# Kernel optimization log

Measured on AMD Instinct MI355X. Metric: run time of the kernel, lower is better.

The kernel has to match this reference:

```python
import jax, jax.numpy as jnp
import numpy as np

N_NODES = 50000
N_EDGES = 1600000
N_FEAT = 512
N_HID = 256
N_CLS = 64
K_HOPS = 10
ALPHA = 0.1


def setup_inputs() -> dict:
    key = jax.random.key(0)
    k1, k2, k3, k4 = jax.random.split(key, 4)
    x = jax.random.normal(k1, (N_NODES, N_FEAT), dtype=jnp.float32)
    edge_index = jax.random.randint(k2, (2, N_EDGES), 0, N_NODES, dtype=jnp.int64)
    W1 = jax.random.normal(k3, (N_HID, N_FEAT), dtype=jnp.float32) * (1.0 / np.sqrt(N_FEAT))
    W2 = jax.random.normal(k4, (N_CLS, N_HID), dtype=jnp.float32) * (1.0 / np.sqrt(N_HID))
    return {"x": x, "edge_index": edge_index, "W1": W1, "W2": W2}


def reference(x, edge_index, W1, W2):
    n = x.shape[0]
    # --- MLP encoder (eval mode: dropout is identity) ---
    hidden = jax.nn.relu(x @ W1.T)            # [N, n_hidden]
    out = hidden @ W2.T                        # [N, n_classes]

    # --- GCN normalization with self-loops (PyG gcn_norm defaults) ---
    loops = jnp.arange(n, dtype=edge_index.dtype)
    src = jnp.concatenate([edge_index[0], loops])  # [E+N]
    dst = jnp.concatenate([edge_index[1], loops])  # [E+N]
    deg = jax.ops.segment_sum(jnp.ones_like(src, dtype=out.dtype), dst, num_segments=n)
    dinv = jnp.where(deg > 0, jax.lax.rsqrt(deg), 0.0)
    norm = dinv[src] * dinv[dst]                   # [E+N]

    # --- APPNP: K hops of propagate + teleport blend ---
    h0 = out
    for _ in range(K_HOPS):
        msg = norm[:, None] * out[src]                         # gather [E+N, C]
        agg = jax.ops.segment_sum(msg, dst, num_segments=n)    # scatter-add [N, C]
        out = (1.0 - ALPHA) * agg + ALPHA * h0

    return jax.nn.log_softmax(out, axis=1)
```

## Files before the change

kernel.cpp:

```cpp
#include <hip/hip_runtime.h>
#include <hip/hip_bf16.h>
#include <cstdint>
#include <cstddef>

#define N_NODES 50000
#define N_EDGES 1600000
#define N_FEAT  512
#define N_HID   256
#define N_CLS   64
#define K_HOPS  10
#define NPAD    50016
#define DUMMY   N_NODES
#define P16(d) (((d) + 15) & ~15)
#define STAGE_CAP 256
#define HOP_GRID 3125
#define NPS 6250

typedef __attribute__((ext_vector_type(4))) float f32x4;
typedef __attribute__((ext_vector_type(4))) int   i32x4;
typedef __attribute__((ext_vector_type(2))) unsigned int u32x2;
typedef __attribute__((ext_vector_type(4))) unsigned short u16x4;
typedef __attribute__((ext_vector_type(8))) short s16x8;

__device__ __forceinline__ ushort f2bf(float f) {
    uint32_t u = __float_as_uint(f);
    uint32_t r = (u + 0x7FFFu + ((u >> 16) & 1u)) >> 16;
    return (ushort)r;
}

__device__ __forceinline__ uint32_t cvtpk(float a, float b) {
    uint32_t r;
    asm("v_cvt_pk_bf16_f32 %0, %1, %2" : "=v"(r) : "v"(a), "v"(b));
    return r;
}

__device__ __forceinline__ f32x4 bf4_to_f32(u16x4 v) {
    f32x4 r;
    r[0] = __uint_as_float((uint32_t)v[0] << 16);
    r[1] = __uint_as_float((uint32_t)v[1] << 16);
    r[2] = __uint_as_float((uint32_t)v[2] << 16);
    r[3] = __uint_as_float((uint32_t)v[3] << 16);
    return r;
}

__global__ void xb_k(const float* __restrict__ X, const float* __restrict__ W1,
                     ushort* __restrict__ Xb, ushort* __restrict__ W1b) {
    const size_t NX = (size_t)N_NODES * N_FEAT;
    const size_t NW = (size_t)N_HID * N_FEAT;
    size_t i = ((size_t)blockIdx.x * 256 + threadIdx.x) * 8;
    if (i < NX) {
        const f32x4 a = *reinterpret_cast<const f32x4*>(X + i);
        const f32x4 b = *reinterpret_cast<const f32x4*>(X + i + 4);
        uint4 o;
        o.x = cvtpk(a[0], a[1]); o.y = cvtpk(a[2], a[3]);
        o.z = cvtpk(b[0], b[1]); o.w = cvtpk(b[2], b[3]);
        *reinterpret_cast<uint4*>(Xb + i) = o;
    } else {
        size_t j = i - NX;
        if (j < NW) {
            const f32x4 a = *reinterpret_cast<const f32x4*>(W1 + j);
            const f32x4 b = *reinterpret_cast<const f32x4*>(W1 + j + 4);
            uint4 o;
            o.x = cvtpk(a[0], a[1]); o.y = cvtpk(a[2], a[3]);
            o.z = cvtpk(b[0], b[1]); o.w = cvtpk(b[2], b[3]);
            *reinterpret_cast<uint4*>(W1b + j) = o;
        }
    }
}

__launch_bounds__(256)
__global__ void gemm1_k(const ushort* __restrict__ Xb, const ushort* __restrict__ W1b,
                        ushort* __restrict__ H) {
    __shared__ ushort sA[128 * 64];
    __shared__ ushort sB[128 * 64];
    const int m0 = blockIdx.x * 128;
    const int n0 = blockIdx.y * 128;
    const int t = threadIdx.x;
    const int wid = t >> 6, lane = t & 63;
    const int wr = wid >> 1, wc = wid & 1;
    const int lo = lane & 15, hi = lane >> 4;

    f32x4 acc[4][4] = {};

    for (int kt = 0; kt < N_FEAT; kt += 64) {
        #pragma unroll
        for (int p = 0; p < 4; ++p) {
            int idx = p * 256 + t;
            int row = idx >> 3, g = idx & 7;
            int grow = m0 + row; if (grow > N_NODES - 1) grow = N_NODES - 1;
            uint4 v = *reinterpret_cast<const uint4*>(Xb + (size_t)grow * N_FEAT + kt + g * 8);
            *reinterpret_cast<uint4*>(&sA[row * 64 + ((g ^ (row & 7)) << 3)]) = v;
        }
        #pragma unroll
        for (int p = 0; p < 4; ++p) {
            int idx = p * 256 + t;
            int row = idx >> 3, g = idx & 7;
            uint4 v = *reinterpret_cast<const uint4*>(W1b + (size_t)(n0 + row) * N_FEAT + kt + g * 8);
            *reinterpret_cast<uint4*>(&sB[row * 64 + ((g ^ (row & 7)) << 3)]) = v;
        }
        __syncthreads();
        #pragma unroll
        for (int kk = 0; kk < 2; ++kk) {
            const int g = kk * 4 + hi;
            s16x8 a[4], b[4];
            #pragma unroll
            for (int i = 0; i < 4; ++i) {
                int row = wr * 64 + i * 16 + lo;
                a[i] = *reinterpret_cast<const s16x8*>(&sA[row * 64 + ((g ^ (row & 7)) << 3)]);
            }
            #pragma unroll
            for (int j = 0; j < 4; ++j) {
                int row = wc * 64 + j * 16 + lo;
                b[j] = *reinterpret_cast<const s16x8*>(&sB[row * 64 + ((g ^ (row & 7)) << 3)]);
            }
            #pragma unroll
            for (int i = 0; i < 4; ++i)
                #pragma unroll
                for (int j = 0; j < 4; ++j)
                    acc[i][j] = __builtin_amdgcn_mfma_f32_16x16x32_bf16(a[i], b[j], acc[i][j], 0, 0, 0);
        }
        __syncthreads();
    }
    #pragma unroll
    for (int i = 0; i < 4; ++i) {
        int rbase = m0 + wr * 64 + i * 16 + hi * 4;
        #pragma unroll
        for (int j = 0; j < 4; ++j) {
            int col = n0 + wc * 64 + j * 16 + lo;
            #pragma unroll
            for (int r = 0; r < 4; ++r) {
                int row = rbase + r;
                if (row < N_NODES) {
                    float v = acc[i][j][r];
                    H[(size_t)row * N_HID + col] = f2bf(fmaxf(v, 0.0f));
                }
            }
        }
    }
}

__launch_bounds__(256)
__global__ void gemm2_k(const ushort* __restrict__ H, const float* __restrict__ W2,
                        const float* __restrict__ dinv, ushort* __restrict__ out) {
    __shared__ ushort sA[128 * 64];
    __shared__ ushort sB[64 * 64];
    const int m0 = blockIdx.x * 128;
    const int t = threadIdx.x;
    const int wid = t >> 6, lane = t & 63;
    const int lo = lane & 15, hi = lane >> 4;

    f32x4 acc[2][4] = {};

    for (int kt = 0; kt < N_HID; kt += 64) {
        #pragma unroll
        for (int p = 0; p < 4; ++p) {
            int idx = p * 256 + t;
            int row = idx >> 3, g = idx & 7;
            int grow = m0 + row; if (grow > N_NODES - 1) grow = N_NODES - 1;
            uint4 v = *reinterpret_cast<const uint4*>(H + (size_t)grow * N_HID + kt + g * 8);
            *reinterpret_cast<uint4*>(&sA[row * 64 + ((g ^ (row & 7)) << 3)]) = v;
        }
        #pragma unroll
        for (int p = 0; p < 4; ++p) {
            int idx = p * 256 + t;
            int row = idx >> 4, f4 = idx & 15;
            const float4 v = *reinterpret_cast<const float4*>(W2 + (size_t)row * N_HID + kt + f4 * 4);
            uint2 h; h.x = cvtpk(v.x, v.y); h.y = cvtpk(v.z, v.w);
            int g = f4 >> 1;
            int off = row * 64 + ((g ^ (row & 7)) << 3) + ((f4 & 1) << 2);
            *reinterpret_cast<uint2*>(&sB[off]) = h;
        }
        __syncthreads();
        #pragma unroll
        for (int kk = 0; kk < 2; ++kk) {
            const int g = kk * 4 + hi;
            s16x8 a[2], b[4];
            #pragma unroll
            for (int i = 0; i < 2; ++i) {
                int row = wid * 32 + i * 16 + lo;
                a[i] = *reinterpret_cast<const s16x8*>(&sA[row * 64 + ((g ^ (row & 7)) << 3)]);
            }
            #pragma unroll
            for (int j = 0; j < 4; ++j) {
                int row = j * 16 + lo;
                b[j] = *reinterpret_cast<const s16x8*>(&sB[row * 64 + ((g ^ (row & 7)) << 3)]);
            }
            #pragma unroll
            for (int i = 0; i < 2; ++i)
                #pragma unroll
                for (int j = 0; j < 4; ++j)
                    acc[i][j] = __builtin_amdgcn_mfma_f32_16x16x32_bf16(a[i], b[j], acc[i][j], 0, 0, 0);
        }
        __syncthreads();
    }
    #pragma unroll
    for (int i = 0; i < 2; ++i) {
        int rbase = m0 + wid * 32 + i * 16 + hi * 4;
        #pragma unroll
        for (int r = 0; r < 4; ++r) {
            int row = rbase + r;
            if (row < N_NODES) {
                const float dv = dinv[row];
                #pragma unroll
                for (int j = 0; j < 4; ++j)
                    out[(size_t)row * 64 + j * 16 + lo] = f2bf(acc[i][j][r] * dv);
            }
        }
    }
}

__global__ void deg_k(const int* __restrict__ dst, int* __restrict__ deg) {
    int e = (blockIdx.x * 256 + threadIdx.x) * 4;
    if (e + 3 < N_EDGES) {
        const i32x4 d = __builtin_nontemporal_load(
            reinterpret_cast<const i32x4*>(dst + e));
        atomicAdd(&deg[d[0]], 1);
        atomicAdd(&deg[d[1]], 1);
        atomicAdd(&deg[d[2]], 1);
        atomicAdd(&deg[d[3]], 1);
    } else {
        for (int k = 0; k < 4 && e + k < N_EDGES; ++k)
            atomicAdd(&deg[dst[e + k]], 1);
    }
}

__global__ void dinv_k(const int* __restrict__ deg, float* __restrict__ dinv,
                       float* __restrict__ rd) {
    int n = blockIdx.x * 256 + threadIdx.x;
    if (n < N_NODES) {
        float dp1 = (float)deg[n] + 1.0f;
        dinv[n] = rsqrtf(dp1);
        rd[n]   = sqrtf(dp1);
    }
}

__device__ __forceinline__ int wave_incl_scan(int v, int lane) {
    #pragma unroll
    for (int d = 1; d < 64; d <<= 1) {
        int u = __shfl_up(v, d, 64);
        if (lane >= d) v += u;
    }
    return v;
}

__global__ void scan_p1(const int* __restrict__ cnt, int* __restrict__ partial) {
    int i = blockIdx.x * 256 + threadIdx.x;
    int v = (i < N_NODES) ? P16(cnt[i]) : 0;
    #pragma unroll
    for (int d = 32; d; d >>= 1) v += __shfl_xor(v, d, 64);
    __shared__ int wt[4];
    int wid = threadIdx.x >> 6, lane = threadIdx.x & 63;
    if (lane == 0) wt[wid] = v;
    __syncthreads();
    if (threadIdx.x == 0) partial[blockIdx.x] = wt[0] + wt[1] + wt[2] + wt[3];
}

__global__ void scan_p2(const int* __restrict__ partial, int* __restrict__ chunkoff,
                        int* __restrict__ row_ptr) {
    int t = threadIdx.x;
    int v = (t < 196) ? partial[t] : 0;
    int lane = t & 63, wid = t >> 6;
    int incl = wave_incl_scan(v, lane);
    __shared__ int wt[4];
    if (lane == 63) wt[wid] = incl;
    __syncthreads();
    int woff = 0;
    for (int w = 0; w < wid; ++w) woff += wt[w];
    int excl = incl - v + woff;
    if (t < 196) chunkoff[t] = excl;
    if (t == 0) row_ptr[N_NODES] = wt[0] + wt[1] + wt[2] + wt[3];
}

__global__ void scan_p3(const int* __restrict__ cnt, const int* __restrict__ chunkoff,
                        int* __restrict__ row_ptr) {
    int i = blockIdx.x * 256 + threadIdx.x;
    int v = (i < N_NODES) ? P16(cnt[i]) : 0;
    int lane = threadIdx.x & 63, wid = threadIdx.x >> 6;
    int incl = wave_incl_scan(v, lane);
    __shared__ int wt[4];
    if (lane == 63) wt[wid] = incl;
    __syncthreads();
    int woff = 0;
    for (int w = 0; w < wid; ++w) woff += wt[w];
    int excl = incl - v + woff;
    if (i < N_NODES) row_ptr[i] = chunkoff[blockIdx.x] + excl;
}

__global__ void scatter_k(const int* __restrict__ src, const int* __restrict__ dst,
                          const int* __restrict__ row_ptr,
                          int* __restrict__ cursor, int* __restrict__ csr) {
    const int slice = blockIdx.x & 7;
    const int lo = slice * NPS;
    int e = ((blockIdx.x >> 3) * 256 + threadIdx.x) * 4;
    if (e + 3 < N_EDGES) {
        const i32x4 d4 = __builtin_nontemporal_load(
            reinterpret_cast<const i32x4*>(dst + e));
        const i32x4 s4 = __builtin_nontemporal_load(
            reinterpret_cast<const i32x4*>(src + e));
        #pragma unroll
        for (int k = 0; k < 4; ++k) {
            const int d = d4[k];
            if ((unsigned)(d - lo) < (unsigned)NPS) {
                int pos = atomicAdd(&cursor[d], 1);
                csr[row_ptr[d] + pos] = s4[k];
            }
        }
    } else {
        for (int k = 0; k < 4 && e + k < N_EDGES; ++k) {
            int d = dst[e + k];
            if ((unsigned)(d - lo) < (unsigned)NPS) {
                int pos = atomicAdd(&cursor[d], 1);
                csr[row_ptr[d] + pos] = src[e + k];
            }
        }
    }
}

__global__ void padfill_k(const int* __restrict__ deg, const int* __restrict__ row_ptr,
                          int* __restrict__ csr) {
    int n = blockIdx.x * 256 + threadIdx.x;
    if (n >= N_NODES) return;
    int d = deg[n];
    int base = row_ptr[n] + d;
    int pad = P16(d) - d;
    for (int i = 0; i < pad; ++i) csr[base + i] = DUMMY;
}

__global__ void zdum_k(ushort* __restrict__ b0, ushort* __restrict__ b1,
                       ushort* __restrict__ b2) {
    int t = threadIdx.x;
    if (t >= 192) return;
    ushort* b = (t < 64) ? b0 : (t < 128) ? b1 : b2;
    int w = t & 63;
    b[(size_t)DUMMY * 64 + w] = 0;
}

__launch_bounds__(256)
__global__ void hop_k(const ushort* __restrict__ prev, const ushort* __restrict__ h0,
                      ushort* __restrict__ next, const int* __restrict__ csr,
                      const int* __restrict__ row_ptr, const float* __restrict__ dinv) {
    __shared__ int scsr[4][STAGE_CAP];
    const int bid = blockIdx.x;
    const int wid = threadIdx.x >> 6;
    const int lane = threadIdx.x & 63;
    const int nb = bid * 16 + wid * 4;
    const int slot = lane >> 4;
    const int cq = (lane & 15) << 2;

    const int b0 = __builtin_amdgcn_readfirstlane(row_ptr[nb]);
    const int e0 = __builtin_amdgcn_readfirstlane(row_ptr[nb + 1]);
    const int e1 = __builtin_amdgcn_readfirstlane(row_ptr[nb + 2]);
    const int e2 = __builtin_amdgcn_readfirstlane(row_ptr[nb + 3]);
    const int e3 = __builtin_amdgcn_readfirstlane(row_ptr[nb + 4]);
    const int tot = e3 - b0;

    int* sw = scsr[wid];
    #pragma unroll
    for (int k = 0; k < 4; ++k) {
        int off = k * 64 + lane;
        if (off < tot && off < STAGE_CAP)
            sw[off] = __builtin_nontemporal_load(csr + b0 + off);
    }

    f32x4 a0 = {0.f,0.f,0.f,0.f}, a1 = a0, a2 = a0, a3 = a0;

#define NODE_LOOP(Bg, Eg, ACC)                                                   \
    {                                                                            \
        int ib = (Bg);                                                           \
        for (; ib + 32 <= (Eg); ib += 32) {                                      \
            int s[8];                                                            \
            if (ib + 32 - b0 <= STAGE_CAP) {                                     \
                int base = ib - b0 + slot;                                       \
                _Pragma("unroll")                                                \
                for (int k = 0; k < 8; ++k) s[k] = sw[base + 4 * k];             \
            } else {                                                             \
                _Pragma("unroll")                                                \
                for (int k = 0; k < 8; ++k)                                      \
                    s[k] = __builtin_nontemporal_load(csr + ib + slot + 4 * k);  \
            }                                                                    \
            u16x4 p[8];                                                          \
            _Pragma("unroll")                                                    \
            for (int k = 0; k < 8; ++k)                                          \
                p[k] = *reinterpret_cast<const u16x4*>(prev + (size_t)s[k] * 64 + cq); \
            _Pragma("unroll")                                                    \
            for (int k = 0; k < 8; ++k) {                                        \
                const f32x4 f = bf4_to_f32(p[k]);                                \
                ACC[0] += f[0]; ACC[1] += f[1]; ACC[2] += f[2]; ACC[3] += f[3];  \
            }                                                                    \
        }                                                                        \
        if (ib < (Eg)) {                                                         \
            int s[4];                                                            \
            if (ib + 16 - b0 <= STAGE_CAP) {                                     \
                int base = ib - b0 + slot;                                       \
                _Pragma("unroll")                                                \
                for (int k = 0; k < 4; ++k) s[k] = sw[base + 4 * k];             \
            } else {                                                             \
                _Pragma("unroll")                                                \
                for (int k = 0; k < 4; ++k)                                      \
                    s[k] = __builtin_nontemporal_load(csr + ib + slot + 4 * k);  \
            }                                                                    \
            u16x4 p[4];                                                          \
            _Pragma("unroll")                                                    \
            for (int k = 0; k < 4; ++k)                                          \
                p[k] = *reinterpret_cast<const u16x4*>(prev + (size_t)s[k] * 64 + cq); \
            _Pragma("unroll")                                                    \
            for (int k = 0; k < 4; ++k) {                                        \
                const f32x4 f = bf4_to_f32(p[k]);                                \
                ACC[0] += f[0]; ACC[1] += f[1]; ACC[2] += f[2]; ACC[3] += f[3];  \
            }                                                                    \
        }                                                                        \
    }

    NODE_LOOP(b0, e0, a0)
    NODE_LOOP(e0, e1, a1)
    NODE_LOOP(e1, e2, a2)
    NODE_LOOP(e2, e3, a3)
#undef NODE_LOOP

    #pragma unroll
    for (int c = 0; c < 4; ++c) {
        a0[c] += __shfl_xor(a0[c], 16, 64); a0[c] += __shfl_xor(a0[c], 32, 64);
        a1[c] += __shfl_xor(a1[c], 16, 64); a1[c] += __shfl_xor(a1[c], 32, 64);
        a2[c] += __shfl_xor(a2[c], 16, 64); a2[c] += __shfl_xor(a2[c], 32, 64);
        a3[c] += __shfl_xor(a3[c], 16, 64); a3[c] += __shfl_xor(a3[c], 32, 64);
    }

    {
        const int node = nb + slot;
        const float di = dinv[node];
        const float di2 = di * di;
        f32x4 av = a0;
        if (slot == 1) av = a1;
        if (slot == 2) av = a2;
        if (slot == 3) av = a3;
        const size_t off = (size_t)node * 64 + cq;
        const f32x4 pv = bf4_to_f32(*reinterpret_cast<const u16x4*>(prev + off));
        const f32x4 hh = bf4_to_f32(__builtin_nontemporal_load(
            reinterpret_cast<const u16x4*>(h0 + off)));
        float r0 = 0.9f * di2 * (av[0] + pv[0]) + 0.1f * hh[0];
        float r1 = 0.9f * di2 * (av[1] + pv[1]) + 0.1f * hh[1];
        float r2 = 0.9f * di2 * (av[2] + pv[2]) + 0.1f * hh[2];
        float r3 = 0.9f * di2 * (av[3] + pv[3]) + 0.1f * hh[3];
        u32x2 o;
        o[0] = cvtpk(r0, r1);
        o[1] = cvtpk(r2, r3);
        __builtin_nontemporal_store(o, reinterpret_cast<u32x2*>(next + off));
    }
}

__launch_bounds__(256)
__global__ void logsm_k(const ushort* __restrict__ in, const float* __restrict__ rd,
                        float* __restrict__ out) {
    int r = (blockIdx.x * 256 + threadIdx.x) >> 6;
    int lane = threadIdx.x & 63;
    if (r >= N_NODES) return;
    float v = __uint_as_float((uint32_t)in[(size_t)r * 64 + lane] << 16) * rd[r];
    float m = v;
    #pragma unroll
    for (int d = 32; d; d >>= 1) m = fmaxf(m, __shfl_xor(m, d, 64));
    float e = __expf(v - m);
    float s = e;
    #pragma unroll
    for (int d = 32; d; d >>= 1) s += __shfl_xor(s, d, 64);
    out[(size_t)r * N_CLS + lane] = (v - m) - __logf(s);
}

extern "C" void kernel_launch(void* const* d_in, const int* in_sizes, int n_in,
                              void* d_out, int out_size, void* d_ws, size_t ws_size,
                              hipStream_t stream) {
    const float* X  = (const float*)d_in[0];
    const int*   EI = (const int*)d_in[1];
    const float* W1 = (const float*)d_in[2];
    const float* W2 = (const float*)d_in[3];
    const int* src = EI;
    const int* dst = EI + N_EDGES;

    char* ws = (char*)d_ws;
    ushort* Xb     = (ushort*)(ws + 0);
    ushort* W1b    = (ushort*)(ws + 51200000);
    ushort* H      = (ushort*)(ws + 51462144);
    ushort* h0t    = (ushort*)(ws + 0);
    ushort* pp0    = (ushort*)(ws + 6402048);
    ushort* pp1    = (ushort*)(ws + 12804096);
    int*    csr    = (int*)  (ws + 19206144);
    int*    deg    = (int*)  (ws + 28806144);
    float*  dinv   = (float*)(ws + 29006144);
    float*  rd     = (float*)(ws + 29206144);
    int*    rptr   = (int*)  (ws + 29406144);
    int*    cursor = (int*)  (ws + 29606148);
    int*    part   = (int*)  (ws + 29806148);
    int*    coff   = (int*)  (ws + 29806932);

    xb_k<<<12564, 256, 0, stream>>>(X, W1, Xb, W1b);
    gemm1_k<<<dim3(391, 2), 256, 0, stream>>>(Xb, W1b, H);

    hipMemsetAsync(deg, 0, N_NODES * sizeof(int), stream);
    hipMemsetAsync(cursor, 0, N_NODES * sizeof(int), stream);
    deg_k<<<1563, 256, 0, stream>>>(dst, deg);
    dinv_k<<<196, 256, 0, stream>>>(deg, dinv, rd);
    scan_p1<<<196, 256, 0, stream>>>(deg, part);
    scan_p2<<<1, 256, 0, stream>>>(part, coff, rptr);
    scan_p3<<<196, 256, 0, stream>>>(deg, coff, rptr);
    scatter_k<<<12504, 256, 0, stream>>>(src, dst, rptr, cursor, csr);
    padfill_k<<<196, 256, 0, stream>>>(deg, rptr, csr);

    gemm2_k<<<391, 256, 0, stream>>>(H, W2, dinv, h0t);
    zdum_k<<<1, 256, 0, stream>>>(h0t, pp0, pp1);

    const ushort* p = h0t;
    ushort* bufs[2] = {pp0, pp1};
    for (int k = 0; k < K_HOPS; ++k) {
        ushort* nx = bufs[k & 1];
        hop_k<<<HOP_GRID, 256, 0, stream>>>(p, h0t, nx, csr, rptr, dinv);
        p = nx;
    }
    logsm_k<<<12500, 256, 0, stream>>>(p, rd, (float*)d_out);
}
```

Measured before the change: 492.4 us.

## Record per-edge slot from degree atomics and drop second atomic pass in CSR build

The degree-counting kernel now keeps the value returned by each atomicAdd as that edge's slot within its destination row and stores it to a per-edge array. The scatter kernel then writes each source index directly at row_ptr[dst]+slot. This removes the second round of atomics, the cursor array and its memset, and the 8-way destination slicing that re-read the edge list eight times. The cost is an extra 6.4 MB per-edge array that is written once and read once, plus non-temporal stores in the degree kernel.

```diff
diff --git a/kernel.cpp b/kernel.cpp
--- a/kernel.cpp
+++ b/kernel.cpp
@@ -14,7 +14,6 @@
 #define P16(d) (((d) + 15) & ~15)
 #define STAGE_CAP 256
 #define HOP_GRID 3125
-#define NPS 6250
 
 typedef __attribute__((ext_vector_type(4))) float f32x4;
 typedef __attribute__((ext_vector_type(4))) int   i32x4;
@@ -209,18 +208,21 @@
     }
 }
 
-__global__ void deg_k(const int* __restrict__ dst, int* __restrict__ deg) {
+__global__ void deg_k(const int* __restrict__ dst, int* __restrict__ deg,
+                      int* __restrict__ pos) {
     int e = (blockIdx.x * 256 + threadIdx.x) * 4;
     if (e + 3 < N_EDGES) {
         const i32x4 d = __builtin_nontemporal_load(
             reinterpret_cast<const i32x4*>(dst + e));
-        atomicAdd(&deg[d[0]], 1);
-        atomicAdd(&deg[d[1]], 1);
-        atomicAdd(&deg[d[2]], 1);
-        atomicAdd(&deg[d[3]], 1);
+        i32x4 p;
+        p[0] = atomicAdd(&deg[d[0]], 1);
+        p[1] = atomicAdd(&deg[d[1]], 1);
+        p[2] = atomicAdd(&deg[d[2]], 1);
+        p[3] = atomicAdd(&deg[d[3]], 1);
+        __builtin_nontemporal_store(p, reinterpret_cast<i32x4*>(pos + e));
     } else {
         for (int k = 0; k < 4 && e + k < N_EDGES; ++k)
-            atomicAdd(&deg[dst[e + k]], 1);
+            pos[e + k] = atomicAdd(&deg[dst[e + k]], 1);
     }
 }
 
@@ -287,32 +289,22 @@
 }
 
 __global__ void scatter_k(const int* __restrict__ src, const int* __restrict__ dst,
-                          const int* __restrict__ row_ptr,
-                          int* __restrict__ cursor, int* __restrict__ csr) {
-    const int slice = blockIdx.x & 7;
-    const int lo = slice * NPS;
-    int e = ((blockIdx.x >> 3) * 256 + threadIdx.x) * 4;
+                          const int* __restrict__ pos, const int* __restrict__ row_ptr,
+                          int* __restrict__ csr) {
+    int e = (blockIdx.x * 256 + threadIdx.x) * 4;
     if (e + 3 < N_EDGES) {
         const i32x4 d4 = __builtin_nontemporal_load(
             reinterpret_cast<const i32x4*>(dst + e));
         const i32x4 s4 = __builtin_nontemporal_load(
             reinterpret_cast<const i32x4*>(src + e));
-        #pragma unroll
-        for (int k = 0; k < 4; ++k) {
-            const int d = d4[k];
-            if ((unsigned)(d - lo) < (unsigned)NPS) {
-                int pos = atomicAdd(&cursor[d], 1);
-                csr[row_ptr[d] + pos] = s4[k];
-            }
-        }
+        const i32x4 p4 = __builtin_nontemporal_load(
+            reinterpret_cast<const i32x4*>(pos + e));
+        #pragma unroll
+        for (int k = 0; k < 4; ++k)
+            csr[row_ptr[d4[k]] + p4[k]] = s4[k];
     } else {
-        for (int k = 0; k < 4 && e + k < N_EDGES; ++k) {
-            int d = dst[e + k];
-            if ((unsigned)(d - lo) < (unsigned)NPS) {
-                int pos = atomicAdd(&cursor[d], 1);
-                csr[row_ptr[d] + pos] = src[e + k];
-            }
-        }
+        for (int k = 0; k < 4 && e + k < N_EDGES; ++k)
+            csr[row_ptr[dst[e + k]] + pos[e + k]] = src[e + k];
     }
 }
 
@@ -487,21 +479,20 @@
     float*  dinv   = (float*)(ws + 29006144);
     float*  rd     = (float*)(ws + 29206144);
     int*    rptr   = (int*)  (ws + 29406144);
-    int*    cursor = (int*)  (ws + 29606148);
-    int*    part   = (int*)  (ws + 29806148);
-    int*    coff   = (int*)  (ws + 29806932);
+    int*    part   = (int*)  (ws + 29606148);
+    int*    coff   = (int*)  (ws + 29606932);
+    int*    pos    = (int*)  (ws + 29607744);
 
     xb_k<<<12564, 256, 0, stream>>>(X, W1, Xb, W1b);
     gemm1_k<<<dim3(391, 2), 256, 0, stream>>>(Xb, W1b, H);
 
     hipMemsetAsync(deg, 0, N_NODES * sizeof(int), stream);
-    hipMemsetAsync(cursor, 0, N_NODES * sizeof(int), stream);
-    deg_k<<<1563, 256, 0, stream>>>(dst, deg);
+    deg_k<<<1563, 256, 0, stream>>>(dst, deg, pos);
     dinv_k<<<196, 256, 0, stream>>>(deg, dinv, rd);
     scan_p1<<<196, 256, 0, stream>>>(deg, part);
     scan_p2<<<1, 256, 0, stream>>>(part, coff, rptr);
     scan_p3<<<196, 256, 0, stream>>>(deg, coff, rptr);
-    scatter_k<<<12504, 256, 0, stream>>>(src, dst, rptr, cursor, csr);
+    scatter_k<<<1563, 256, 0, stream>>>(src, dst, pos, rptr, csr);
     padfill_k<<<196, 256, 0, stream>>>(deg, rptr, csr);
 
     gemm2_k<<<391, 256, 0, stream>>>(H, W2, dinv, h0t);
```

New measurement: 452.3 us. 1.09x faster.
